# Kernel tuning notes

Measured on AMD Instinct MI355X. Metric: run time of the kernel, lower is better.

The kernel has to match this reference:

```python
import jax, jax.numpy as jnp
import numpy as np

B, S, HID = 2, 2048, 2048
NH, NKV, HD = 16, 16, 128
SCALE = 1.0 / np.sqrt(HD)


def _rotate_half(x):
    x1, x2 = jnp.split(x, 2, axis=-1)
    return jnp.concatenate([-x2, x1], axis=-1)


def setup_inputs() -> dict:
    key = jax.random.key(0)
    k1, k2, k3 = jax.random.split(key, 3)
    hidden_states = jax.random.normal(k1, (B, S, HID), dtype=jnp.float32)
    # standard RoPE cos/sin tables, shape [S, HD]
    inv_freq = 1.0 / (10000.0 ** (np.arange(0, HD, 2, dtype=np.float32) / HD))
    freqs = np.outer(np.arange(S, dtype=np.float32), inv_freq)  # [S, HD/2]
    emb = np.concatenate([freqs, freqs], axis=-1)               # [S, HD]
    cos = jnp.asarray(np.cos(emb), dtype=jnp.float32)
    sin = jnp.asarray(np.sin(emb), dtype=jnp.float32)
    # torch Linear weights are [out, in]; forward computes x @ W.T
    w_qkv = jax.random.normal(k2, ((NH + 2 * NKV) * HD, HID), dtype=jnp.float32) * 0.02
    w_o = jax.random.normal(k3, (HID, NH * HD), dtype=jnp.float32) * 0.02
    return {"hidden_states": hidden_states, "cos": cos, "sin": sin,
            "w_qkv": w_qkv, "w_o": w_o}


def reference(hidden_states, cos, sin, w_qkv, w_o):
    b, s, _ = hidden_states.shape
    qkv = hidden_states @ w_qkv.T                         # [B,S,(NH+2*NKV)*HD]
    qkv = qkv.reshape(b, s, NH + 2 * NKV, HD)
    q = qkv[:, :, :NH]                                    # [B,S,NH,HD]
    k = qkv[:, :, NH:NH + NKV]                            # [B,S,NKV,HD]
    v = qkv[:, :, NH + NKV:]                              # [B,S,NKV,HD]
    # RoPE: broadcast cos/sin [S,HD] -> [1,S,1,HD]
    c = cos[None, :, None, :]
    sn = sin[None, :, None, :]
    q = q * c + _rotate_half(q) * sn
    k = k * c + _rotate_half(k) * sn
    scores = jnp.einsum("bihd,bjhd->bhij", q, k) * SCALE  # [B,H,S,S]
    attn = jax.nn.softmax(scores, axis=-1)
    out = jnp.einsum("bhij,bjhd->bihd", attn, v)          # [B,S,H,HD]
    out = out.reshape(b, s, NH * HD)
    return out @ w_o.T                                    # [B,S,HID]
```

## Files before the change

### kernel.cpp

```cpp
#include <hip/hip_runtime.h>
#include <hip/hip_bf16.h>

typedef float f32x4 __attribute__((ext_vector_type(4)));
typedef __bf16 bf16x8 __attribute__((ext_vector_type(8)));
typedef __bf16 bf16x4 __attribute__((ext_vector_type(4)));

#define S_LEN 2048
#define NHEADS 16
#define HDIM 128
#define KLOG2E (0.08838834764831845f * 1.4426950408889634f)
#define MSHIFT 2.0f

__device__ __forceinline__ void gld_lds16(const __bf16* g, __bf16* l) {
  __builtin_amdgcn_global_load_lds(
      (__attribute__((address_space(1))) void*)(void*)g,
      (__attribute__((address_space(3))) void*)l,
      16, 0, 0);
}

template <int N>
__device__ __forceinline__ void waitv() {
  if constexpr (N == 8)      asm volatile("s_waitcnt vmcnt(8)" ::: "memory");
  else if constexpr (N == 6) asm volatile("s_waitcnt vmcnt(6)" ::: "memory");
  else if constexpr (N == 4) asm volatile("s_waitcnt vmcnt(4)" ::: "memory");
  else if constexpr (N == 3) asm volatile("s_waitcnt vmcnt(3)" ::: "memory");
  else                       asm volatile("s_waitcnt vmcnt(0)" ::: "memory");
}

__global__ __launch_bounds__(256) void cvt_f32_bf16(const float* __restrict__ in,
                                                    __bf16* __restrict__ out, int n) {
  int i = (blockIdx.x * 256 + threadIdx.x) * 4;
  if (i >= n) return;
  float4 v = *(const float4*)(in + i);
  bf16x4 o;
  o[0] = (__bf16)v.x; o[1] = (__bf16)v.y; o[2] = (__bf16)v.z; o[3] = (__bf16)v.w;
  *(bf16x4*)(out + i) = o;
}

template <int MREP>
__device__ __forceinline__ void gemm_core(const __bf16* __restrict__ A,
                                          const __bf16* __restrict__ B,
                                          __bf16* lds, int am0, int bn0,
                                          f32x4 (&acc)[MREP][4]) {
  constexpr int K = 2048;
  constexpr int AF = MREP * 2;
  constexpr int SLOT = (AF + 16) * 512;
  constexpr int NA = AF / 8;
  constexpr int NL = NA + 2;
  const int tid = threadIdx.x;
  const int w = tid >> 6, lane = tid & 63;
  const int l15 = lane & 15;
  const int wm = w >> 2, wn = w & 3;

  const __bf16* asrc = A + (size_t)(am0 + l15) * K + (lane >> 4) * 8;
  const __bf16* bsrc = B + (size_t)(bn0 + l15) * K + (lane >> 4) * 8;

  auto stage = [&](int t) {
    __bf16* s = lds + (t & 3) * SLOT;
#pragma unroll
    for (int i = 0; i < NA; ++i) {
      const int f = w * NA + i;
      gld_lds16(asrc + (size_t)f * (16 * K) + t * 32, s + f * 512 + lane * 8);
    }
#pragma unroll
    for (int i = 0; i < 2; ++i) {
      const int g = w * 2 + i;
      gld_lds16(bsrc + (size_t)g * (16 * K) + t * 32, s + (AF + g) * 512 + lane * 8);
    }
  };

  stage(0); stage(1); stage(2);
  waitv<2 * NL>();
  __builtin_amdgcn_s_barrier();

  for (int t = 0; t < 64; ++t) {
    if (t < 61) stage(t + 3);
    const __bf16* s = lds + (t & 3) * SLOT + lane * 8;
    const __bf16* sB = s + AF * 512;
    bf16x8 bfr[4];
#pragma unroll
    for (int j = 0; j < 4; ++j)
      bfr[j] = *(const bf16x8*)(sB + (wn * 4 + j) * 512);
#pragma unroll
    for (int half = 0; half < MREP / 4; ++half) {
      bf16x8 af[4];
#pragma unroll
      for (int i = 0; i < 4; ++i)
        af[i] = *(const bf16x8*)(s + (wm * MREP + half * 4 + i) * 512);
      __builtin_amdgcn_s_setprio(1);
#pragma unroll
      for (int i = 0; i < 4; ++i)
#pragma unroll
        for (int j = 0; j < 4; ++j)
          acc[half * 4 + i][j] = __builtin_amdgcn_mfma_f32_16x16x32_bf16(
              af[i], bfr[j], acc[half * 4 + i][j], 0, 0, 0);
      __builtin_amdgcn_s_setprio(0);
    }
    if (t < 63) {
      if (t < 61)      waitv<2 * NL>();
      else if (t == 61) waitv<NL>();
      else             waitv<0>();
      __builtin_amdgcn_s_barrier();
    }
  }
}


__global__ __launch_bounds__(512)
void gemm_bt_qkp(const __bf16* __restrict__ A, const __bf16* __restrict__ B,
                 __bf16* __restrict__ Qp, __bf16* __restrict__ Kp) {
  __shared__ alignas(16) __bf16 lds[4 * 32 * 512];
  const int am0 = blockIdx.y * 256;
  const int bn0 = blockIdx.x * 256;
  const int tid = threadIdx.x;
  const int w = tid >> 6, lane = tid & 63;
  const int l15 = lane & 15, quad = lane >> 4;
  const int wm = w >> 2, wn = w & 3;
  f32x4 acc[8][4] = {};
  gemm_core<8>(A, B, lds, am0, bn0, acc);
#pragma unroll
  for (int i = 0; i < 8; ++i) {
    const int row_b = am0 + wm * 128 + i * 16 + quad * 4;
    const int b = row_b >> 11;
    const int s = row_b & 2047;
    const int s16 = s >> 4;
    const int l15p0 = s & 15;
#pragma unroll
    for (int j = 0; j < 4; ++j) {
      const int col = bn0 + wn * 64 + j * 16 + l15;
      const int head = col >> 7;
      const int h = head & 15;
      const int d = col & 127;
      const int kk = d >> 5, quadp = (d >> 3) & 3, e = d & 7;
      __bf16* dst = (head < 16) ? Qp : Kp;
      size_t base = (((size_t)((b * 16 + h) * 128 + s16) * 4 + kk) * 64
                     + quadp * 16 + l15p0) * 8 + e;
#pragma unroll
      for (int r = 0; r < 4; ++r)
        dst[base + (size_t)r * 8] = (__bf16)acc[i][j][r];
    }
  }
}

__global__ __launch_bounds__(512)
void gemm_bt_vp(const __bf16* __restrict__ A, const __bf16* __restrict__ B,
                __bf16* __restrict__ Vp) {
  __shared__ alignas(16) __bf16 lds[4 * 24 * 512];
  const int am0 = blockIdx.y * 128;
  const int bn0 = blockIdx.x * 256;
  const int tid = threadIdx.x;
  const int w = tid >> 6, lane = tid & 63;
  const int l15 = lane & 15, quad = lane >> 4;
  const int wm = w >> 2, wn = w & 3;
  f32x4 acc[4][4] = {};
  gemm_core<4>(A, B, lds, am0, bn0, acc);
#pragma unroll
  for (int i = 0; i < 4; ++i) {
    const int row_b = am0 + wm * 64 + i * 16 + quad * 4;
    const int b = row_b >> 11;
    const int key0 = row_b & 2047;
    const int quadp = (key0 >> 3) & 3;
    const int kkv = key0 >> 5;
    const int e0 = key0 & 7;
#pragma unroll
    for (int j = 0; j < 4; ++j) {
      const int col = bn0 + wn * 64 + j * 16 + l15;
      const int h = col >> 7, dd = col & 127;
      const int tt = dd >> 4, l15p = dd & 15;
      bf16x4 o;
#pragma unroll
      for (int r = 0; r < 4; ++r) o[r] = (__bf16)acc[i][j][r];
      size_t addr = (((size_t)((b * 16 + h) * 8 + tt) * 64 + kkv) * 64
                     + quadp * 16 + l15p) * 8 + e0;
      *(bf16x4*)(Vp + addr) = o;
    }
  }
}

__global__ __launch_bounds__(512)
void gemm_bt_f(const __bf16* __restrict__ A, const __bf16* __restrict__ B,
               float* __restrict__ C) {
  __shared__ alignas(16) __bf16 lds[4 * 24 * 512];
  const int am0 = blockIdx.y * 128;
  const int bn0 = blockIdx.x * 256;
  const int tid = threadIdx.x;
  const int w = tid >> 6, lane = tid & 63;
  const int l15 = lane & 15, quad = lane >> 4;
  const int wm = w >> 2, wn = w & 3;
  f32x4 acc[4][4] = {};
  gemm_core<4>(A, B, lds, am0, bn0, acc);
#pragma unroll
  for (int i = 0; i < 4; ++i) {
    const int row_b = am0 + wm * 64 + i * 16 + quad * 4;
#pragma unroll
    for (int j = 0; j < 4; ++j) {
      const int col = bn0 + wn * 64 + j * 16 + l15;
#pragma unroll
      for (int r = 0; r < 4; ++r)
        C[(size_t)(row_b + r) * 2048 + col] = acc[i][j][r];
    }
  }
}

__global__ __launch_bounds__(256)
void rope_inplace(__bf16* __restrict__ Qp, __bf16* __restrict__ Kp,
                  const float* __restrict__ cosp, const float* __restrict__ sinp) {
  int t = blockIdx.x * 256 + threadIdx.x;
  int lane = t & 63;
  int kk = (t >> 6) & 1;
  int s16 = (t >> 7) & 127;
  int bh = (t >> 14) & 31;
  __bf16* buf = (t >> 19) ? Kp : Qp;
  int l15 = lane & 15, quad = lane >> 4;
  int s = s16 * 16 + l15;
  int d = kk * 32 + quad * 8;
  size_t base = (((size_t)(bh * 128 + s16) * 4 + kk) * 64 + lane) * 8;
  size_t base2 = base + 2 * 64 * 8;
  bf16x8 x1 = *(bf16x8*)(buf + base);
  bf16x8 x2 = *(bf16x8*)(buf + base2);
  float4 c0 = *(const float4*)(cosp + s * 128 + d);
  float4 c1 = *(const float4*)(cosp + s * 128 + d + 4);
  float4 s0 = *(const float4*)(sinp + s * 128 + d);
  float4 s1 = *(const float4*)(sinp + s * 128 + d + 4);
  float cs[8] = {c0.x, c0.y, c0.z, c0.w, c1.x, c1.y, c1.z, c1.w};
  float sn[8] = {s0.x, s0.y, s0.z, s0.w, s1.x, s1.y, s1.z, s1.w};
  bf16x8 o1, o2;
#pragma unroll
  for (int e = 0; e < 8; ++e) {
    float a = (float)x1[e], bb = (float)x2[e];
    o1[e] = (__bf16)(a * cs[e] - bb * sn[e]);
    o2[e] = (__bf16)(bb * cs[e] + a * sn[e]);
  }
  *(bf16x8*)(buf + base) = o1;
  *(bf16x8*)(buf + base2) = o2;
}

__global__ __launch_bounds__(256)
void attn_kernel(const __bf16* __restrict__ Qp, const __bf16* __restrict__ Kp,
                 const __bf16* __restrict__ Vp, __bf16* __restrict__ O) {
  const int qt = blockIdx.x;
  const int bh = blockIdx.y;
  const int b = bh >> 4, h = bh & 15;
  const int tid = threadIdx.x;
  const int w = tid >> 6;
  const int lane = tid & 63;
  const int l15 = lane & 15, quad = lane >> 4;

  __shared__ alignas(16) __bf16 Kls[2][16 * 512];
  __shared__ alignas(16) __bf16 Vls[2][16 * 512];
  __shared__ alignas(16) __bf16 Ps[4][16][72];

  const __bf16* qbase = Qp + (size_t)bh * 262144 + lane * 8;
  const __bf16* kbase = Kp + (size_t)bh * 262144 + lane * 8;
  const __bf16* vbase = Vp + (size_t)bh * 262144 + lane * 8;

  bf16x8 qf[2][4];
#pragma unroll
  for (int qb = 0; qb < 2; ++qb)
#pragma unroll
    for (int kk = 0; kk < 4; ++kk)
      qf[qb][kk] = *(const bf16x8*)(qbase + (size_t)((qt * 8 + qb * 4 + w) * 4 + kk) * 512);

  bf16x8 onesf;
#pragma unroll
  for (int e = 0; e < 8; ++e) onesf[e] = (__bf16)1.0f;

  f32x4 o_acc[2][8] = {};
  f32x4 o_sum[2] = {};

#pragma unroll
  for (int ii = 0; ii < 4; ++ii) {
    const int c = w * 4 + ii;
    gld_lds16(kbase + (size_t)c * 512, &Kls[0][c * 512 + lane * 8]);
    gld_lds16(vbase + (size_t)((c >> 1) * 64 + (c & 1)) * 512,
              &Vls[0][c * 512 + lane * 8]);
  }
  __syncthreads();

  int cur = 0;
  for (int j0 = 0; j0 < S_LEN; j0 += 64) {
    if (j0 + 64 < S_LEN) {
      const int j16n = (j0 + 64) >> 4;
      const int kvn = (j0 + 64) >> 5;
#pragma unroll
      for (int ii = 0; ii < 4; ++ii) {
        const int c = w * 4 + ii;
        gld_lds16(kbase + (size_t)(j16n * 4 + c) * 512,
                  &Kls[cur ^ 1][c * 512 + lane * 8]);
        gld_lds16(vbase + (size_t)((c >> 1) * 64 + kvn + (c & 1)) * 512,
                  &Vls[cur ^ 1][c * 512 + lane * 8]);
      }
    }

    f32x4 sc[2][4] = {};
    __builtin_amdgcn_s_setprio(1);
#pragma unroll
    for (int kk = 0; kk < 4; ++kk) {
#pragma unroll
      for (int t = 0; t < 4; ++t) {
        bf16x8 kf = *(const bf16x8*)(&Kls[cur][(t * 4 + kk) * 512 + lane * 8]);
        sc[0][t] = __builtin_amdgcn_mfma_f32_16x16x32_bf16(qf[0][kk], kf, sc[0][t], 0, 0, 0);
        sc[1][t] = __builtin_amdgcn_mfma_f32_16x16x32_bf16(qf[1][kk], kf, sc[1][t], 0, 0, 0);
      }
    }
    __builtin_amdgcn_s_setprio(0);

    bf16x8 a[2][2];
#pragma unroll
    for (int qb = 0; qb < 2; ++qb) {
#pragma unroll
      for (int t = 0; t < 4; ++t)
#pragma unroll
        for (int r = 0; r < 4; ++r)
          Ps[w][quad * 4 + r][t * 16 + l15] =
              (__bf16)exp2f(sc[qb][t][r] * KLOG2E - MSHIFT);
      a[qb][0] = *(const bf16x8*)&Ps[w][l15][quad * 8];
      a[qb][1] = *(const bf16x8*)&Ps[w][l15][32 + quad * 8];
    }

    __builtin_amdgcn_s_setprio(1);
#pragma unroll
    for (int kk = 0; kk < 2; ++kk) {
      o_sum[0] = __builtin_amdgcn_mfma_f32_16x16x32_bf16(a[0][kk], onesf, o_sum[0], 0, 0, 0);
      o_sum[1] = __builtin_amdgcn_mfma_f32_16x16x32_bf16(a[1][kk], onesf, o_sum[1], 0, 0, 0);
#pragma unroll
      for (int t = 0; t < 8; ++t) {
        bf16x8 vf = *(const bf16x8*)(&Vls[cur][(t * 2 + kk) * 512 + lane * 8]);
        o_acc[0][t] = __builtin_amdgcn_mfma_f32_16x16x32_bf16(a[0][kk], vf, o_acc[0][t], 0, 0, 0);
        o_acc[1][t] = __builtin_amdgcn_mfma_f32_16x16x32_bf16(a[1][kk], vf, o_acc[1][t], 0, 0, 0);
      }
    }
    __builtin_amdgcn_s_setprio(0);

    __syncthreads();
    cur ^= 1;
  }

#pragma unroll
  for (int qb = 0; qb < 2; ++qb) {
    float inv[4];
#pragma unroll
    for (int r = 0; r < 4; ++r) inv[r] = 1.0f / o_sum[qb][r];
    const int row0 = qt * 128 + (qb * 4 + w) * 16 + quad * 4;
#pragma unroll
    for (int t = 0; t < 8; ++t)
#pragma unroll
      for (int r = 0; r < 4; ++r)
        O[(size_t)(b * S_LEN + row0 + r) * 2048 + h * HDIM + t * 16 + l15] =
            (__bf16)(o_acc[qb][t][r] * inv[r]);
  }
}

extern "C" void kernel_launch(void* const* d_in, const int* in_sizes, int n_in,
                              void* d_out, int out_size, void* d_ws, size_t ws_size,
                              hipStream_t stream) {
  const float* hs   = (const float*)d_in[0];
  const float* cosp = (const float*)d_in[1];
  const float* sinp = (const float*)d_in[2];
  const float* wqkv = (const float*)d_in[3];
  const float* wo   = (const float*)d_in[4];
  float* out = (float*)d_out;

  char* ws = (char*)d_ws;
  __bf16* Xb   = (__bf16*)(ws);
  __bf16* Obuf = (__bf16*)(ws);
  __bf16* Wqb  = (__bf16*)(ws + 16777216);
  __bf16* Wob  = (__bf16*)(ws + 41943040);
  __bf16* Qp   = (__bf16*)(ws + 50331648);
  __bf16* Kp   = (__bf16*)(ws + 67108864);
  __bf16* Vp   = (__bf16*)(ws + 83886080);
  if (ws_size < 100663296) return;

  cvt_f32_bf16<<<8192, 256, 0, stream>>>(hs, Xb, 8388608);
  cvt_f32_bf16<<<12288, 256, 0, stream>>>(wqkv, Wqb, 12582912);
  cvt_f32_bf16<<<4096, 256, 0, stream>>>(wo, Wob, 4194304);

  gemm_bt_qkp<<<dim3(16, 16), 512, 0, stream>>>(Xb, Wqb, Qp, Kp);
  gemm_bt_vp<<<dim3(8, 32), 512, 0, stream>>>(Xb, Wqb + 8388608, Vp);
  rope_inplace<<<4096, 256, 0, stream>>>(Qp, Kp, cosp, sinp);
  attn_kernel<<<dim3(16, 32), 256, 0, stream>>>(Qp, Kp, Vp, Obuf);
  gemm_bt_f<<<dim3(8, 32), 512, 0, stream>>>(Obuf, Wob, out);
}
```

Before: 435.7 us.

## Fuse RoPE into QK GEMM epilogue, merge casts, retile attention with triple buffering

New measurement: 408.1 us. 1.07x faster.

```diff
diff --git a/kernel.cpp b/kernel.cpp
--- a/kernel.cpp
+++ b/kernel.cpp
@@ -27,17 +27,24 @@
   else                       asm volatile("s_waitcnt vmcnt(0)" ::: "memory");
 }
 
-__global__ __launch_bounds__(256) void cvt_f32_bf16(const float* __restrict__ in,
-                                                    __bf16* __restrict__ out, int n) {
+__global__ __launch_bounds__(256)
+void cvt_all(const float* __restrict__ i0, __bf16* __restrict__ o0,
+             const float* __restrict__ i1, __bf16* __restrict__ o1,
+             const float* __restrict__ i2, __bf16* __restrict__ o2) {
   int i = (blockIdx.x * 256 + threadIdx.x) * 4;
-  if (i >= n) return;
-  float4 v = *(const float4*)(in + i);
+  if (i >= 25165824) return;
+  const float* in;
+  __bf16* out;
+  if (i < 8388608)       { in = i0 + i;              out = o0 + i; }
+  else if (i < 20971520) { in = i1 + (i - 8388608);  out = o1 + (i - 8388608); }
+  else                   { in = i2 + (i - 20971520); out = o2 + (i - 20971520); }
+  float4 v = *(const float4*)in;
   bf16x4 o;
   o[0] = (__bf16)v.x; o[1] = (__bf16)v.y; o[2] = (__bf16)v.z; o[3] = (__bf16)v.w;
-  *(bf16x4*)(out + i) = o;
-}
-
-template <int MREP>
+  *(bf16x4*)out = o;
+}
+
+template <int MREP, bool RMAP>
 __device__ __forceinline__ void gemm_core(const __bf16* __restrict__ A,
                                           const __bf16* __restrict__ B,
                                           __bf16* lds, int am0, int bn0,
@@ -79,8 +86,11 @@
     const __bf16* sB = s + AF * 512;
     bf16x8 bfr[4];
 #pragma unroll
-    for (int j = 0; j < 4; ++j)
-      bfr[j] = *(const bf16x8*)(sB + (wn * 4 + j) * 512);
+    for (int j = 0; j < 4; ++j) {
+      const int g = RMAP ? ((wn >> 1) * 8 + (wn & 1) * 2 + (j & 1) + (j >> 1) * 4)
+                         : (wn * 4 + j);
+      bfr[j] = *(const bf16x8*)(sB + g * 512);
+    }
 #pragma unroll
     for (int half = 0; half < MREP / 4; ++half) {
       bf16x8 af[4];
@@ -97,9 +107,9 @@
       __builtin_amdgcn_s_setprio(0);
     }
     if (t < 63) {
-      if (t < 61)      waitv<2 * NL>();
+      if (t < 61)       waitv<2 * NL>();
       else if (t == 61) waitv<NL>();
-      else             waitv<0>();
+      else              waitv<0>();
       __builtin_amdgcn_s_barrier();
     }
   }
@@ -108,8 +118,9 @@
 
 __global__ __launch_bounds__(512)
 void gemm_bt_qkp(const __bf16* __restrict__ A, const __bf16* __restrict__ B,
-                 __bf16* __restrict__ Qp, __bf16* __restrict__ Kp) {
-  __shared__ alignas(16) __bf16 lds[4 * 32 * 512];
+                 __bf16* __restrict__ Qp, __bf16* __restrict__ Kp,
+                 const float* __restrict__ cosp, const float* __restrict__ sinp) {
+  __shared__ alignas(16) char smem[139264];
   const int am0 = blockIdx.y * 256;
   const int bn0 = blockIdx.x * 256;
   const int tid = threadIdx.x;
@@ -117,27 +128,52 @@
   const int l15 = lane & 15, quad = lane >> 4;
   const int wm = w >> 2, wn = w & 3;
   f32x4 acc[8][4] = {};
-  gemm_core<8>(A, B, lds, am0, bn0, acc);
+  gemm_core<8, true>(A, B, (__bf16*)smem, am0, bn0, acc);
+
+  __syncthreads();
+  float* csb = (float*)smem;
+  float* snb = csb + 256 * 68;
+  const int sbase = am0 & 2047;
+  for (int q = tid; q < 4096; q += 512) {
+    const int row = q >> 4, dq = (q & 15) * 4;
+    *(float4*)(csb + row * 68 + dq) =
+        *(const float4*)(cosp + (size_t)(sbase + row) * 128 + dq);
+    *(float4*)(snb + row * 68 + dq) =
+        *(const float4*)(sinp + (size_t)(sbase + row) * 128 + dq);
+  }
+  __syncthreads();
+
+  const int head_sel = wn >> 1;
+  const int hcol0 = bn0 + head_sel * 128;
+  const int head = hcol0 >> 7;
+  const int h = head & 15;
+  __bf16* dst = (head < 16) ? Qp : Kp;
 #pragma unroll
   for (int i = 0; i < 8; ++i) {
     const int row_b = am0 + wm * 128 + i * 16 + quad * 4;
-    const int b = row_b >> 11;
+    const int bidx = row_b >> 11;
     const int s = row_b & 2047;
+    const int sl = wm * 128 + i * 16 + quad * 4;
     const int s16 = s >> 4;
     const int l15p0 = s & 15;
 #pragma unroll
-    for (int j = 0; j < 4; ++j) {
-      const int col = bn0 + wn * 64 + j * 16 + l15;
-      const int head = col >> 7;
-      const int h = head & 15;
-      const int d = col & 127;
-      const int kk = d >> 5, quadp = (d >> 3) & 3, e = d & 7;
-      __bf16* dst = (head < 16) ? Qp : Kp;
-      size_t base = (((size_t)((b * 16 + h) * 128 + s16) * 4 + kk) * 64
-                     + quadp * 16 + l15p0) * 8 + e;
-#pragma unroll
-      for (int r = 0; r < 4; ++r)
-        dst[base + (size_t)r * 8] = (__bf16)acc[i][j][r];
+    for (int j2 = 0; j2 < 2; ++j2) {
+      const int dl = (wn & 1) * 32 + j2 * 16 + l15;
+      const int dh = dl + 64;
+      const int kkl = dl >> 5, qpl = (dl >> 3) & 3, el = dl & 7;
+      const int kkh = dh >> 5, qph = (dh >> 3) & 3, eh = dh & 7;
+      const size_t base_lo =
+          (((size_t)((bidx * 16 + h) * 128 + s16) * 4 + kkl) * 64 + qpl * 16 + l15p0) * 8 + el;
+      const size_t base_hi =
+          (((size_t)((bidx * 16 + h) * 128 + s16) * 4 + kkh) * 64 + qph * 16 + l15p0) * 8 + eh;
+#pragma unroll
+      for (int r = 0; r < 4; ++r) {
+        const float c = csb[(sl + r) * 68 + dl];
+        const float sn = snb[(sl + r) * 68 + dl];
+        const float a = acc[i][j2][r], bb = acc[i][j2 + 2][r];
+        dst[base_lo + (size_t)r * 8] = (__bf16)(a * c - bb * sn);
+        dst[base_hi + (size_t)r * 8] = (__bf16)(bb * c + a * sn);
+      }
     }
   }
 }
@@ -153,7 +189,7 @@
   const int l15 = lane & 15, quad = lane >> 4;
   const int wm = w >> 2, wn = w & 3;
   f32x4 acc[4][4] = {};
-  gemm_core<4>(A, B, lds, am0, bn0, acc);
+  gemm_core<4, false>(A, B, lds, am0, bn0, acc);
 #pragma unroll
   for (int i = 0; i < 4; ++i) {
     const int row_b = am0 + wm * 64 + i * 16 + quad * 4;
@@ -188,7 +224,7 @@
   const int l15 = lane & 15, quad = lane >> 4;
   const int wm = w >> 2, wn = w & 3;
   f32x4 acc[4][4] = {};
-  gemm_core<4>(A, B, lds, am0, bn0, acc);
+  gemm_core<4, false>(A, B, lds, am0, bn0, acc);
 #pragma unroll
   for (int i = 0; i < 4; ++i) {
     const int row_b = am0 + wm * 64 + i * 16 + quad * 4;
@@ -202,53 +238,20 @@
   }
 }
 
-__global__ __launch_bounds__(256)
-void rope_inplace(__bf16* __restrict__ Qp, __bf16* __restrict__ Kp,
-                  const float* __restrict__ cosp, const float* __restrict__ sinp) {
-  int t = blockIdx.x * 256 + threadIdx.x;
-  int lane = t & 63;
-  int kk = (t >> 6) & 1;
-  int s16 = (t >> 7) & 127;
-  int bh = (t >> 14) & 31;
-  __bf16* buf = (t >> 19) ? Kp : Qp;
-  int l15 = lane & 15, quad = lane >> 4;
-  int s = s16 * 16 + l15;
-  int d = kk * 32 + quad * 8;
-  size_t base = (((size_t)(bh * 128 + s16) * 4 + kk) * 64 + lane) * 8;
-  size_t base2 = base + 2 * 64 * 8;
-  bf16x8 x1 = *(bf16x8*)(buf + base);
-  bf16x8 x2 = *(bf16x8*)(buf + base2);
-  float4 c0 = *(const float4*)(cosp + s * 128 + d);
-  float4 c1 = *(const float4*)(cosp + s * 128 + d + 4);
-  float4 s0 = *(const float4*)(sinp + s * 128 + d);
-  float4 s1 = *(const float4*)(sinp + s * 128 + d + 4);
-  float cs[8] = {c0.x, c0.y, c0.z, c0.w, c1.x, c1.y, c1.z, c1.w};
-  float sn[8] = {s0.x, s0.y, s0.z, s0.w, s1.x, s1.y, s1.z, s1.w};
-  bf16x8 o1, o2;
-#pragma unroll
-  for (int e = 0; e < 8; ++e) {
-    float a = (float)x1[e], bb = (float)x2[e];
-    o1[e] = (__bf16)(a * cs[e] - bb * sn[e]);
-    o2[e] = (__bf16)(bb * cs[e] + a * sn[e]);
-  }
-  *(bf16x8*)(buf + base) = o1;
-  *(bf16x8*)(buf + base2) = o2;
-}
-
-__global__ __launch_bounds__(256)
+__global__ __launch_bounds__(512)
 void attn_kernel(const __bf16* __restrict__ Qp, const __bf16* __restrict__ Kp,
                  const __bf16* __restrict__ Vp, __bf16* __restrict__ O) {
-  const int qt = blockIdx.x;
-  const int bh = blockIdx.y;
+  const int lid = blockIdx.x;
+  const int qt = (lid >> 3) & 7;
+  const int bh = (lid & 7) * 4 + (lid >> 6);
   const int b = bh >> 4, h = bh & 15;
   const int tid = threadIdx.x;
   const int w = tid >> 6;
   const int lane = tid & 63;
   const int l15 = lane & 15, quad = lane >> 4;
 
-  __shared__ alignas(16) __bf16 Kls[2][16 * 512];
-  __shared__ alignas(16) __bf16 Vls[2][16 * 512];
-  __shared__ alignas(16) __bf16 Ps[4][16][72];
+  __shared__ alignas(16) __bf16 KV[3][32 * 512];
+  __shared__ alignas(16) __bf16 Ps[8][16][72];
 
   const __bf16* qbase = Qp + (size_t)bh * 262144 + lane * 8;
   const __bf16* kbase = Kp + (size_t)bh * 262144 + lane * 8;
@@ -259,7 +262,8 @@
   for (int qb = 0; qb < 2; ++qb)
 #pragma unroll
     for (int kk = 0; kk < 4; ++kk)
-      qf[qb][kk] = *(const bf16x8*)(qbase + (size_t)((qt * 8 + qb * 4 + w) * 4 + kk) * 512);
+      qf[qb][kk] =
+          *(const bf16x8*)(qbase + (size_t)((qt * 16 + qb * 8 + w) * 4 + kk) * 512);
 
   bf16x8 onesf;
 #pragma unroll
@@ -268,39 +272,35 @@
   f32x4 o_acc[2][8] = {};
   f32x4 o_sum[2] = {};
 
-#pragma unroll
-  for (int ii = 0; ii < 4; ++ii) {
-    const int c = w * 4 + ii;
-    gld_lds16(kbase + (size_t)c * 512, &Kls[0][c * 512 + lane * 8]);
-    gld_lds16(vbase + (size_t)((c >> 1) * 64 + (c & 1)) * 512,
-              &Vls[0][c * 512 + lane * 8]);
-  }
-  __syncthreads();
-
-  int cur = 0;
-  for (int j0 = 0; j0 < S_LEN; j0 += 64) {
-    if (j0 + 64 < S_LEN) {
-      const int j16n = (j0 + 64) >> 4;
-      const int kvn = (j0 + 64) >> 5;
-#pragma unroll
-      for (int ii = 0; ii < 4; ++ii) {
-        const int c = w * 4 + ii;
-        gld_lds16(kbase + (size_t)(j16n * 4 + c) * 512,
-                  &Kls[cur ^ 1][c * 512 + lane * 8]);
-        gld_lds16(vbase + (size_t)((c >> 1) * 64 + kvn + (c & 1)) * 512,
-                  &Vls[cur ^ 1][c * 512 + lane * 8]);
-      }
-    }
+  auto stage = [&](int tile) {
+    __bf16* s = &KV[tile % 3][0];
+#pragma unroll
+    for (int ii = 0; ii < 2; ++ii) {
+      const int c = w * 2 + ii;
+      gld_lds16(kbase + ((size_t)tile * 16 + c) * 512, s + c * 512 + lane * 8);
+      gld_lds16(vbase + (size_t)((c >> 1) * 64 + tile * 2 + (c & 1)) * 512,
+                s + (16 + c) * 512 + lane * 8);
+    }
+  };
+
+  stage(0);
+  stage(1);
+  waitv<4>();
+  __builtin_amdgcn_s_barrier();
+
+  for (int t = 0; t < 32; ++t) {
+    if (t + 2 < 32) stage(t + 2);
+    const __bf16* kvs = &KV[t % 3][0] + lane * 8;
 
     f32x4 sc[2][4] = {};
     __builtin_amdgcn_s_setprio(1);
 #pragma unroll
     for (int kk = 0; kk < 4; ++kk) {
 #pragma unroll
-      for (int t = 0; t < 4; ++t) {
-        bf16x8 kf = *(const bf16x8*)(&Kls[cur][(t * 4 + kk) * 512 + lane * 8]);
-        sc[0][t] = __builtin_amdgcn_mfma_f32_16x16x32_bf16(qf[0][kk], kf, sc[0][t], 0, 0, 0);
-        sc[1][t] = __builtin_amdgcn_mfma_f32_16x16x32_bf16(qf[1][kk], kf, sc[1][t], 0, 0, 0);
+      for (int tt = 0; tt < 4; ++tt) {
+        bf16x8 kf = *(const bf16x8*)(kvs + (tt * 4 + kk) * 512);
+        sc[0][tt] = __builtin_amdgcn_mfma_f32_16x16x32_bf16(qf[0][kk], kf, sc[0][tt], 0, 0, 0);
+        sc[1][tt] = __builtin_amdgcn_mfma_f32_16x16x32_bf16(qf[1][kk], kf, sc[1][tt], 0, 0, 0);
       }
     }
     __builtin_amdgcn_s_setprio(0);
@@ -309,11 +309,11 @@
 #pragma unroll
     for (int qb = 0; qb < 2; ++qb) {
 #pragma unroll
-      for (int t = 0; t < 4; ++t)
+      for (int tt = 0; tt < 4; ++tt)
 #pragma unroll
         for (int r = 0; r < 4; ++r)
-          Ps[w][quad * 4 + r][t * 16 + l15] =
-              (__bf16)exp2f(sc[qb][t][r] * KLOG2E - MSHIFT);
+          Ps[w][quad * 4 + r][tt * 16 + l15] =
+              (__bf16)exp2f(sc[qb][tt][r] * KLOG2E - MSHIFT);
       a[qb][0] = *(const bf16x8*)&Ps[w][l15][quad * 8];
       a[qb][1] = *(const bf16x8*)&Ps[w][l15][32 + quad * 8];
     }
@@ -324,16 +324,20 @@
       o_sum[0] = __builtin_amdgcn_mfma_f32_16x16x32_bf16(a[0][kk], onesf, o_sum[0], 0, 0, 0);
       o_sum[1] = __builtin_amdgcn_mfma_f32_16x16x32_bf16(a[1][kk], onesf, o_sum[1], 0, 0, 0);
 #pragma unroll
-      for (int t = 0; t < 8; ++t) {
-        bf16x8 vf = *(const bf16x8*)(&Vls[cur][(t * 2 + kk) * 512 + lane * 8]);
-        o_acc[0][t] = __builtin_amdgcn_mfma_f32_16x16x32_bf16(a[0][kk], vf, o_acc[0][t], 0, 0, 0);
-        o_acc[1][t] = __builtin_amdgcn_mfma_f32_16x16x32_bf16(a[1][kk], vf, o_acc[1][t], 0, 0, 0);
+      for (int tt = 0; tt < 8; ++tt) {
+        bf16x8 vf = *(const bf16x8*)(kvs + (16 + tt * 2 + kk) * 512);
+        o_acc[0][tt] = __builtin_amdgcn_mfma_f32_16x16x32_bf16(a[0][kk], vf, o_acc[0][tt], 0, 0, 0);
+        o_acc[1][tt] = __builtin_amdgcn_mfma_f32_16x16x32_bf16(a[1][kk], vf, o_acc[1][tt], 0, 0, 0);
       }
     }
     __builtin_amdgcn_s_setprio(0);
 
-    __syncthreads();
-    cur ^= 1;
+    if (t < 31) {
+      asm volatile("s_waitcnt lgkmcnt(0)" ::: "memory");
+      if (t < 30) waitv<4>();
+      else        waitv<0>();
+      __builtin_amdgcn_s_barrier();
+    }
   }
 
 #pragma unroll
@@ -341,13 +345,13 @@
     float inv[4];
 #pragma unroll
     for (int r = 0; r < 4; ++r) inv[r] = 1.0f / o_sum[qb][r];
-    const int row0 = qt * 128 + (qb * 4 + w) * 16 + quad * 4;
-#pragma unroll
-    for (int t = 0; t < 8; ++t)
+    const int row0 = qt * 256 + (qb * 8 + w) * 16 + quad * 4;
+#pragma unroll
+    for (int tt = 0; tt < 8; ++tt)
 #pragma unroll
       for (int r = 0; r < 4; ++r)
-        O[(size_t)(b * S_LEN + row0 + r) * 2048 + h * HDIM + t * 16 + l15] =
-            (__bf16)(o_acc[qb][t][r] * inv[r]);
+        O[(size_t)(b * S_LEN + row0 + r) * 2048 + h * HDIM + tt * 16 + l15] =
+            (__bf16)(o_acc[qb][tt][r] * inv[r]);
   }
 }
 
@@ -371,13 +375,10 @@
   __bf16* Vp   = (__bf16*)(ws + 83886080);
   if (ws_size < 100663296) return;
 
-  cvt_f32_bf16<<<8192, 256, 0, stream>>>(hs, Xb, 8388608);
-  cvt_f32_bf16<<<12288, 256, 0, stream>>>(wqkv, Wqb, 12582912);
-  cvt_f32_bf16<<<4096, 256, 0, stream>>>(wo, Wob, 4194304);
-
-  gemm_bt_qkp<<<dim3(16, 16), 512, 0, stream>>>(Xb, Wqb, Qp, Kp);
+  cvt_all<<<24576, 256, 0, stream>>>(hs, Xb, wqkv, Wqb, wo, Wob);
+
+  gemm_bt_qkp<<<dim3(16, 16), 512, 0, stream>>>(Xb, Wqb, Qp, Kp, cosp, sinp);
   gemm_bt_vp<<<dim3(8, 32), 512, 0, stream>>>(Xb, Wqb + 8388608, Vp);
-  rope_inplace<<<4096, 256, 0, stream>>>(Qp, Kp, cosp, sinp);
-  attn_kernel<<<dim3(16, 32), 256, 0, stream>>>(Qp, Kp, Vp, Obuf);
+  attn_kernel<<<256, 512, 0, stream>>>(Qp, Kp, Vp, Obuf);
   gemm_bt_f<<<dim3(8, 32), 512, 0, stream>>>(Obuf, Wob, out);
 }
```
